# Performance work log

Measured on AMD Instinct MI355X. Metric: run time of the kernel, lower is better.

The kernel has to match this reference:

```python
import jax, jax.numpy as jnp
import numpy as np

B, S, D, H, E, K = 4, 1024, 1024, 4096, 8, 2

def setup_inputs() -> dict:
    key = jax.random.key(0)
    ks = jax.random.split(key, 6)
    sd = 1.0 / np.sqrt(D)
    sh = 1.0 / np.sqrt(H)
    return {
        "x": jax.random.normal(ks[0], (B, S, D), jnp.float32),
        "Wg": jax.random.normal(ks[1], (D, E), jnp.float32) * sd,
        "bg": jnp.zeros((E,), jnp.float32),
        "W1": jax.random.normal(ks[2], (E, D, H), jnp.float32) * sd,
        "b1": jnp.zeros((E, H), jnp.float32),
        "Wa": jax.random.normal(ks[3], (E, D, H), jnp.float32) * sd,
        "ba": jnp.zeros((E, H), jnp.float32),
        "W2": jax.random.normal(ks[4], (E, H, D), jnp.float32) * sh,
        "b2": jnp.zeros((E, D), jnp.float32),
        "kv_cache": 0,
    }

def reference(x, Wg, bg, W1, b1, Wa, ba, W2, b2, kv_cache):
    # gate: softmax over experts, top-k, renormalize
    gate = jax.nn.softmax(x @ Wg + bg, axis=-1)            # [B,S,E]
    w, idx = jax.lax.top_k(gate, K)                        # [B,S,K]
    w = w / jnp.sum(w, axis=-1, keepdims=True)
    # dense all-expert FF with SwiGLU: fc2( silu(fc_a(x)) * fc1(x) )
    a = jnp.einsum('bsd,edh->bseh', x, Wa) + ba            # [B,S,E,H]
    g = a * jax.nn.sigmoid(a)
    u = jnp.einsum('bsd,edh->bseh', x, W1) + b1
    y = jnp.einsum('bseh,ehd->bsed', g * u, W2) + b2       # [B,S,E,D]
    # gather top-k experts per token and combine
    sel = jnp.take_along_axis(y, idx[..., None], axis=2)   # [B,S,K,D]
    out = jnp.sum(sel * w[..., None], axis=-2)             # [B,S,D]
    return out
```

## Files before the change

### kernel.cpp

```cpp
#include <hip/hip_runtime.h>
#include <hip/hip_bf16.h>
#include <math.h>

#define TOKENS 4096
#define DD 1024
#define HH 4096
#define NE 8
#define PAIRS 8192
#define ROWCAP 8320
#define TILE_CAP 72

typedef __bf16 bf16x8 __attribute__((ext_vector_type(8)));
typedef float f32x4 __attribute__((ext_vector_type(4)));

__device__ __forceinline__ unsigned short f2bf(float f) {
  union { float f; unsigned int u; } c; c.f = f;
  unsigned int x = c.u;
  return (unsigned short)((x + 0x7fffu + ((x >> 16) & 1u)) >> 16);
}

__device__ __forceinline__ void lds16(void* l, const void* g) {
  __builtin_amdgcn_global_load_lds((const __attribute__((address_space(1))) void*)g,
                                   (__attribute__((address_space(3))) void*)l, 16, 0, 0);
}

__global__ void init_kernel(int* counts) {
  if (threadIdx.x < NE) counts[threadIdx.x] = 0;
}

__global__ __launch_bounds__(256) void transpose_kernel(const float* __restrict__ in,
                                                        unsigned short* __restrict__ out,
                                                        int R, int C) {
  int ntr = R >> 6, ntc = C >> 6;
  int per_e = ntr * ntc;
  int b = blockIdx.x;
  int e = b / per_e;
  int rem = b - e * per_e;
  int tr = rem / ntc, tc = rem - (rem / ntc) * ntc;
  const float* ie = in + (size_t)e * R * C;
  unsigned short* oe = out + (size_t)e * R * C;

  __shared__ float t[64][68];
  int tid = threadIdx.x;
  int lr = tid >> 2;
  int c4 = (tid & 3) << 4;
  const float* src = ie + (size_t)(tr * 64 + lr) * C + tc * 64 + c4;
  float4 v0 = *(const float4*)(src);
  float4 v1 = *(const float4*)(src + 4);
  float4 v2 = *(const float4*)(src + 8);
  float4 v3 = *(const float4*)(src + 12);
  *(float4*)&t[lr][c4] = v0;
  *(float4*)&t[lr][c4 + 4] = v1;
  *(float4*)&t[lr][c4 + 8] = v2;
  *(float4*)&t[lr][c4 + 12] = v3;
  __syncthreads();

  int oc = tid >> 2;
  int r0 = (tid & 3) << 4;
  unsigned int pk[8];
#pragma unroll
  for (int i = 0; i < 8; i++) {
    unsigned int lo = f2bf(t[r0 + 2 * i][oc]);
    unsigned int hi = f2bf(t[r0 + 2 * i + 1][oc]);
    pk[i] = lo | (hi << 16);
  }
  unsigned short* dst = oe + (size_t)(tc * 64 + oc) * R + tr * 64 + r0;
  *(uint4*)(dst) = make_uint4(pk[0], pk[1], pk[2], pk[3]);
  *(uint4*)(dst + 8) = make_uint4(pk[4], pk[5], pk[6], pk[7]);
}

__global__ __launch_bounds__(256) void gate_kernel(const float* __restrict__ x,
    const float* __restrict__ Wg, const float* __restrict__ bg,
    int* __restrict__ counts, int* __restrict__ tok_e, int* __restrict__ tok_slot,
    float* __restrict__ tok_w) {
  int t = blockIdx.x, tid = threadIdx.x;
  const float* xr = x + (size_t)t * DD;
  float p[8] = {0, 0, 0, 0, 0, 0, 0, 0};
  for (int d = tid; d < DD; d += 256) {
    float xv = xr[d];
    const float4* wrow = (const float4*)(Wg + (size_t)d * NE);
    float4 w0 = wrow[0], w1 = wrow[1];
    p[0] += xv * w0.x; p[1] += xv * w0.y; p[2] += xv * w0.z; p[3] += xv * w0.w;
    p[4] += xv * w1.x; p[5] += xv * w1.y; p[6] += xv * w1.z; p[7] += xv * w1.w;
  }
#pragma unroll
  for (int e = 0; e < 8; e++) {
    p[e] += __shfl_down(p[e], 32);
    p[e] += __shfl_down(p[e], 16);
    p[e] += __shfl_down(p[e], 8);
    p[e] += __shfl_down(p[e], 4);
    p[e] += __shfl_down(p[e], 2);
    p[e] += __shfl_down(p[e], 1);
  }
  __shared__ float red[4][8];
  if ((tid & 63) == 0) {
#pragma unroll
    for (int e = 0; e < 8; e++) red[tid >> 6][e] = p[e];
  }
  __syncthreads();
  if (tid == 0) {
    float l[8];
#pragma unroll
    for (int e = 0; e < 8; e++) l[e] = red[0][e] + red[1][e] + red[2][e] + red[3][e] + bg[e];
    int e0 = 0; float l0 = l[0];
    for (int e = 1; e < 8; e++) if (l[e] > l0) { e0 = e; l0 = l[e]; }
    int e1 = -1; float l1 = -3.4e38f;
    for (int e = 0; e < 8; e++) if (e != e0 && l[e] > l1) { e1 = e; l1 = l[e]; }
    float w0 = 1.f / (1.f + __expf(l1 - l0));
    float w1 = 1.f - w0;
    int s0 = atomicAdd(&counts[e0], 1);
    int s1 = atomicAdd(&counts[e1], 1);
    tok_e[2 * t] = e0;     tok_slot[2 * t] = s0;     tok_w[2 * t] = w0;
    tok_e[2 * t + 1] = e1; tok_slot[2 * t + 1] = s1; tok_w[2 * t + 1] = w1;
  }
}

__global__ void scan_kernel(const int* __restrict__ counts, int* __restrict__ offsets,
                            int* __restrict__ tm_e, int* __restrict__ tm_row0,
                            int* __restrict__ tm_nrow, int* __restrict__ ntp) {
  if (threadIdx.x != 0 || blockIdx.x != 0) return;
  int off = 0, nt = 0;
  for (int e = 0; e < NE; e++) {
    offsets[e] = off;
    int c = counts[e];
    for (int r = 0; r < c; r += 128) {
      tm_e[nt] = e;
      tm_row0[nt] = off + r;
      tm_nrow[nt] = (c - r < 128) ? (c - r) : 128;
      nt++;
    }
    off += c;
  }
  *ntp = nt;
}

__global__ __launch_bounds__(64) void gather_kernel(const float* __restrict__ x,
    const int* __restrict__ tok_e, const int* __restrict__ tok_slot,
    const float* __restrict__ tok_w, const int* __restrict__ offsets,
    unsigned short* __restrict__ Xe, int* __restrict__ pair_row, float* __restrict__ rw) {
  int pp = blockIdx.x, tid = threadIdx.x;
  int e = tok_e[pp];
  int row = offsets[e] + tok_slot[pp];
  int t = pp >> 1;
  const float* src = x + (size_t)t * DD + tid * 16;
  float4 v0 = *(const float4*)(src);
  float4 v1 = *(const float4*)(src + 4);
  float4 v2 = *(const float4*)(src + 8);
  float4 v3 = *(const float4*)(src + 12);
  unsigned int pk[8];
  pk[0] = f2bf(v0.x) | ((unsigned int)f2bf(v0.y) << 16);
  pk[1] = f2bf(v0.z) | ((unsigned int)f2bf(v0.w) << 16);
  pk[2] = f2bf(v1.x) | ((unsigned int)f2bf(v1.y) << 16);
  pk[3] = f2bf(v1.z) | ((unsigned int)f2bf(v1.w) << 16);
  pk[4] = f2bf(v2.x) | ((unsigned int)f2bf(v2.y) << 16);
  pk[5] = f2bf(v2.z) | ((unsigned int)f2bf(v2.w) << 16);
  pk[6] = f2bf(v3.x) | ((unsigned int)f2bf(v3.y) << 16);
  pk[7] = f2bf(v3.z) | ((unsigned int)f2bf(v3.w) << 16);
  unsigned short* dst = Xe + (size_t)row * DD + tid * 16;
  *(uint4*)(dst) = make_uint4(pk[0], pk[1], pk[2], pk[3]);
  *(uint4*)(dst + 8) = make_uint4(pk[4], pk[5], pk[6], pk[7]);
  if (tid == 0) { pair_row[pp] = row; rw[row] = tok_w[pp]; }
}

__global__ __launch_bounds__(256) void gemm1_kernel(
    const unsigned short* __restrict__ Xe,
    const unsigned short* __restrict__ WaT,
    const unsigned short* __restrict__ W1T,
    const float* __restrict__ ba, const float* __restrict__ b1,
    unsigned short* __restrict__ h,
    const int* __restrict__ tm_e, const int* __restrict__ tm_row0,
    const int* __restrict__ tm_nrow, const int* __restrict__ ntp) {
  int tile = blockIdx.x >> 6;
  if (tile >= *ntp) return;
  int n0 = (blockIdx.x & 63) << 6;
  int e = tm_e[tile], row0 = tm_row0[tile], nrow = tm_nrow[tile];

  __shared__ unsigned short lA[128 * 32];
  __shared__ unsigned short lBa[64 * 32];
  __shared__ unsigned short lBu[64 * 32];

  int tid = threadIdx.x;
  int lane = tid & 63, wid = tid >> 6;
  int wm = wid >> 1, wn = wid & 1;
  int fr = lane & 15, kc = lane >> 4;

  const unsigned short* gA = Xe + (size_t)row0 * DD;
  const unsigned short* gBa = WaT + ((size_t)e << 22) + (size_t)n0 * DD;
  const unsigned short* gBu = W1T + ((size_t)e << 22) + (size_t)n0 * DD;

  int ar0 = tid >> 2;
  int akc = (tid & 3) << 3;

  f32x4 accA[4][2], accU[4][2];
  f32x4 z = {0.f, 0.f, 0.f, 0.f};
#pragma unroll
  for (int m = 0; m < 4; m++)
#pragma unroll
    for (int n = 0; n < 2; n++) { accA[m][n] = z; accU[m][n] = z; }

  for (int k0 = 0; k0 < DD; k0 += 32) {
    lds16(lA + (size_t)tid * 8,        gA + (size_t)ar0 * DD + k0 + akc);
    lds16(lA + (size_t)(tid + 256) * 8, gA + (size_t)(ar0 + 64) * DD + k0 + akc);
    lds16(lBa + (size_t)tid * 8,       gBa + (size_t)ar0 * DD + k0 + akc);
    lds16(lBu + (size_t)tid * 8,       gBu + (size_t)ar0 * DD + k0 + akc);
    __syncthreads();
    bf16x8 a[4], bA[2], bU[2];
#pragma unroll
    for (int m = 0; m < 4; m++)
      a[m] = *(const bf16x8*)(lA + (wm * 64 + m * 16 + fr) * 32 + kc * 8);
#pragma unroll
    for (int n = 0; n < 2; n++) {
      bA[n] = *(const bf16x8*)(lBa + (wn * 32 + n * 16 + fr) * 32 + kc * 8);
      bU[n] = *(const bf16x8*)(lBu + (wn * 32 + n * 16 + fr) * 32 + kc * 8);
    }
#pragma unroll
    for (int m = 0; m < 4; m++)
#pragma unroll
      for (int n = 0; n < 2; n++) {
        accA[m][n] = __builtin_amdgcn_mfma_f32_16x16x32_bf16(a[m], bA[n], accA[m][n], 0, 0, 0);
        accU[m][n] = __builtin_amdgcn_mfma_f32_16x16x32_bf16(a[m], bU[n], accU[m][n], 0, 0, 0);
      }
    __syncthreads();
  }

  int lr4 = kc * 4;
#pragma unroll
  for (int n = 0; n < 2; n++) {
    int col = n0 + wn * 32 + n * 16 + fr;
    float bav = ba[e * HH + col];
    float buv = b1[e * HH + col];
#pragma unroll
    for (int m = 0; m < 4; m++) {
#pragma unroll
      for (int j = 0; j < 4; j++) {
        int r = wm * 64 + m * 16 + lr4 + j;
        if (r < nrow) {
          float av = accA[m][n][j] + bav;
          float uv = accU[m][n][j] + buv;
          float s = __builtin_amdgcn_rcpf(1.f + __expf(-av));
          float hv = av * s * uv;
          h[(size_t)(row0 + r) * HH + col] = f2bf(hv);
        }
      }
    }
  }
}

__global__ __launch_bounds__(256) void gemm2_kernel(
    const unsigned short* __restrict__ h,
    const unsigned short* __restrict__ W2T,
    const float* __restrict__ b2, const float* __restrict__ rw,
    float* __restrict__ contrib,
    const int* __restrict__ tm_e, const int* __restrict__ tm_row0,
    const int* __restrict__ tm_nrow, const int* __restrict__ ntp) {
  int tile = blockIdx.x >> 3;
  if (tile >= *ntp) return;
  int n0 = (blockIdx.x & 7) << 7;
  int e = tm_e[tile], row0 = tm_row0[tile], nrow = tm_nrow[tile];

  __shared__ unsigned short lA[128 * 32];
  __shared__ unsigned short lB[128 * 32];

  int tid = threadIdx.x;
  int lane = tid & 63, wid = tid >> 6;
  int wm = wid >> 1, wn = wid & 1;
  int fr = lane & 15, kc = lane >> 4;

  const unsigned short* gA = h + (size_t)row0 * HH;
  const unsigned short* gB = W2T + ((size_t)e << 22) + (size_t)n0 * HH;

  int ar0 = tid >> 2;
  int akc = (tid & 3) << 3;

  f32x4 acc[4][4];
  f32x4 z = {0.f, 0.f, 0.f, 0.f};
#pragma unroll
  for (int m = 0; m < 4; m++)
#pragma unroll
    for (int n = 0; n < 4; n++) acc[m][n] = z;

  for (int k0 = 0; k0 < HH; k0 += 32) {
    lds16(lA + (size_t)tid * 8,         gA + (size_t)ar0 * HH + k0 + akc);
    lds16(lA + (size_t)(tid + 256) * 8, gA + (size_t)(ar0 + 64) * HH + k0 + akc);
    lds16(lB + (size_t)tid * 8,         gB + (size_t)ar0 * HH + k0 + akc);
    lds16(lB + (size_t)(tid + 256) * 8, gB + (size_t)(ar0 + 64) * HH + k0 + akc);
    __syncthreads();
    bf16x8 a[4], b[4];
#pragma unroll
    for (int m = 0; m < 4; m++)
      a[m] = *(const bf16x8*)(lA + (wm * 64 + m * 16 + fr) * 32 + kc * 8);
#pragma unroll
    for (int n = 0; n < 4; n++)
      b[n] = *(const bf16x8*)(lB + (wn * 64 + n * 16 + fr) * 32 + kc * 8);
#pragma unroll
    for (int m = 0; m < 4; m++)
#pragma unroll
      for (int n = 0; n < 4; n++)
        acc[m][n] = __builtin_amdgcn_mfma_f32_16x16x32_bf16(a[m], b[n], acc[m][n], 0, 0, 0);
    __syncthreads();
  }

  float b2v[4];
#pragma unroll
  for (int n = 0; n < 4; n++) b2v[n] = b2[e * DD + n0 + wn * 64 + n * 16 + fr];
  int lr4 = kc * 4;
#pragma unroll
  for (int m = 0; m < 4; m++) {
#pragma unroll
    for (int j = 0; j < 4; j++) {
      int r = wm * 64 + m * 16 + lr4 + j;
      if (r < nrow) {
        float wv = rw[row0 + r];
        float* dst = contrib + (size_t)(row0 + r) * DD + n0 + wn * 64 + fr;
#pragma unroll
        for (int n = 0; n < 4; n++)
          dst[n * 16] = wv * (acc[m][n][j] + b2v[n]);
      }
    }
  }
}

__global__ __launch_bounds__(256) void combine_kernel(const float* __restrict__ contrib,
    const int* __restrict__ pair_row, float* __restrict__ out) {
  int t = blockIdx.x, tid = threadIdx.x;
  int r0 = pair_row[2 * t], r1 = pair_row[2 * t + 1];
  const float4* c0 = (const float4*)(contrib + (size_t)r0 * DD);
  const float4* c1 = (const float4*)(contrib + (size_t)r1 * DD);
  float4* o = (float4*)(out + (size_t)t * DD);
  float4 a = c0[tid], b = c1[tid];
  o[tid] = make_float4(a.x + b.x, a.y + b.y, a.z + b.z, a.w + b.w);
}

extern "C" void kernel_launch(void* const* d_in, const int* in_sizes, int n_in,
                              void* d_out, int out_size, void* d_ws, size_t ws_size,
                              hipStream_t stream) {
  const float* x  = (const float*)d_in[0];
  const float* Wg = (const float*)d_in[1];
  const float* bg = (const float*)d_in[2];
  const float* W1 = (const float*)d_in[3];
  const float* b1 = (const float*)d_in[4];
  const float* Wa = (const float*)d_in[5];
  const float* ba = (const float*)d_in[6];
  const float* W2 = (const float*)d_in[7];
  const float* b2 = (const float*)d_in[8];
  float* out = (float*)d_out;
  (void)in_sizes; (void)n_in; (void)out_size; (void)ws_size;

  char* p = (char*)d_ws;
  auto take = [&](size_t bytes) { char* r = p; p += (bytes + 255) & ~(size_t)255; return r; };
  unsigned short* WaT = (unsigned short*)take((size_t)NE * HH * DD * 2);
  unsigned short* W1T = (unsigned short*)take((size_t)NE * HH * DD * 2);
  unsigned short* W2T = (unsigned short*)take((size_t)NE * DD * HH * 2);
  unsigned short* Xe  = (unsigned short*)take((size_t)ROWCAP * DD * 2);
  unsigned short* hb  = (unsigned short*)take((size_t)ROWCAP * HH * 2);
  float* contrib      = (float*)take((size_t)ROWCAP * DD * 4);
  int* counts   = (int*)take(64);
  int* offsets  = (int*)take(64);
  int* tok_e    = (int*)take(PAIRS * 4);
  int* tok_slot = (int*)take(PAIRS * 4);
  float* tok_w  = (float*)take(PAIRS * 4);
  int* pair_row = (int*)take(PAIRS * 4);
  float* rw     = (float*)take(ROWCAP * 4);
  int* tm_e     = (int*)take(TILE_CAP * 4);
  int* tm_row0  = (int*)take(TILE_CAP * 4);
  int* tm_nrow  = (int*)take(TILE_CAP * 4);
  int* ntp      = (int*)take(64);

  init_kernel<<<1, 64, 0, stream>>>(counts);
  transpose_kernel<<<NE * 16 * 64, 256, 0, stream>>>(Wa, WaT, DD, HH);
  transpose_kernel<<<NE * 16 * 64, 256, 0, stream>>>(W1, W1T, DD, HH);
  transpose_kernel<<<NE * 64 * 16, 256, 0, stream>>>(W2, W2T, HH, DD);
  gate_kernel<<<TOKENS, 256, 0, stream>>>(x, Wg, bg, counts, tok_e, tok_slot, tok_w);
  scan_kernel<<<1, 64, 0, stream>>>(counts, offsets, tm_e, tm_row0, tm_nrow, ntp);
  gather_kernel<<<PAIRS, 64, 0, stream>>>(x, tok_e, tok_slot, tok_w, offsets, Xe, pair_row, rw);
  gemm1_kernel<<<TILE_CAP * 64, 256, 0, stream>>>(Xe, WaT, W1T, ba, b1, hb, tm_e, tm_row0, tm_nrow, ntp);
  gemm2_kernel<<<TILE_CAP * 8, 256, 0, stream>>>(hb, W2T, b2, rw, contrib, tm_e, tm_row0, tm_nrow, ntp);
  combine_kernel<<<TOKENS, 256, 0, stream>>>(contrib, pair_row, out);
}
```

Baseline: 563.4 us.

## Enlarge expert GEMM tiles to 256 rows with double-buffered LDS pipeline

Expert row tiles grow from 128 to 256 rows, and both grouped GEMMs move to 512-thread blocks. gemm1 now covers 128 output columns per block. Both kernels use two dynamic-LDS buffers so global-to-LDS loads for the next K step overlap MFMA work on the current one, with explicit waitcnt and barrier in place of __syncthreads. Block indices are remapped to group work across the grid for cache locality. The aims are more weight reuse per load and hidden load latency, at the cost of more padded rows on partial tiles, fewer blocks, and higher register and LDS use per block.

```diff
diff --git a/kernel.cpp b/kernel.cpp
--- a/kernel.cpp
+++ b/kernel.cpp
@@ -7,8 +7,8 @@
 #define HH 4096
 #define NE 8
 #define PAIRS 8192
-#define ROWCAP 8320
-#define TILE_CAP 72
+#define ROWCAP 8448
+#define TILE_CAP 40
 
 typedef __bf16 bf16x8 __attribute__((ext_vector_type(8)));
 typedef float f32x4 __attribute__((ext_vector_type(4)));
@@ -119,17 +119,19 @@
                             int* __restrict__ tm_e, int* __restrict__ tm_row0,
                             int* __restrict__ tm_nrow, int* __restrict__ ntp) {
   if (threadIdx.x != 0 || blockIdx.x != 0) return;
+  int c[NE];
+#pragma unroll
+  for (int e = 0; e < NE; e++) c[e] = counts[e];
   int off = 0, nt = 0;
   for (int e = 0; e < NE; e++) {
     offsets[e] = off;
-    int c = counts[e];
-    for (int r = 0; r < c; r += 128) {
+    for (int r = 0; r < c[e]; r += 256) {
       tm_e[nt] = e;
       tm_row0[nt] = off + r;
-      tm_nrow[nt] = (c - r < 128) ? (c - r) : 128;
+      tm_nrow[nt] = (c[e] - r < 256) ? (c[e] - r) : 256;
       nt++;
     }
-    off += c;
+    off += c[e];
   }
   *ntp = nt;
 }
@@ -162,7 +164,7 @@
   if (tid == 0) { pair_row[pp] = row; rw[row] = tok_w[pp]; }
 }
 
-__global__ __launch_bounds__(256) void gemm1_kernel(
+__global__ __launch_bounds__(512, 2) void gemm1_kernel(
     const unsigned short* __restrict__ Xe,
     const unsigned short* __restrict__ WaT,
     const unsigned short* __restrict__ W1T,
@@ -170,57 +172,65 @@
     unsigned short* __restrict__ h,
     const int* __restrict__ tm_e, const int* __restrict__ tm_row0,
     const int* __restrict__ tm_nrow, const int* __restrict__ ntp) {
-  int tile = blockIdx.x >> 6;
+  extern __shared__ unsigned short sm[];
+  int chunk = gridDim.x >> 3;
+  int work = (blockIdx.x & 7) * chunk + (blockIdx.x >> 3);
+  int tile = work >> 5;
   if (tile >= *ntp) return;
-  int n0 = (blockIdx.x & 63) << 6;
+  int n0 = (work & 31) << 7;
   int e = tm_e[tile], row0 = tm_row0[tile], nrow = tm_nrow[tile];
-
-  __shared__ unsigned short lA[128 * 32];
-  __shared__ unsigned short lBa[64 * 32];
-  __shared__ unsigned short lBu[64 * 32];
 
   int tid = threadIdx.x;
   int lane = tid & 63, wid = tid >> 6;
-  int wm = wid >> 1, wn = wid & 1;
+  int wm = wid >> 2, wn = wid & 3;
   int fr = lane & 15, kc = lane >> 4;
 
   const unsigned short* gA = Xe + (size_t)row0 * DD;
   const unsigned short* gBa = WaT + ((size_t)e << 22) + (size_t)n0 * DD;
   const unsigned short* gBu = W1T + ((size_t)e << 22) + (size_t)n0 * DD;
 
-  int ar0 = tid >> 2;
-  int akc = (tid & 3) << 3;
-
-  f32x4 accA[4][2], accU[4][2];
+  int sr = tid >> 2;
+  int sk = (tid & 3) << 3;
+
+  f32x4 accA[8][2], accU[8][2];
   f32x4 z = {0.f, 0.f, 0.f, 0.f};
 #pragma unroll
-  for (int m = 0; m < 4; m++)
+  for (int m = 0; m < 8; m++)
 #pragma unroll
     for (int n = 0; n < 2; n++) { accA[m][n] = z; accU[m][n] = z; }
 
-  for (int k0 = 0; k0 < DD; k0 += 32) {
-    lds16(lA + (size_t)tid * 8,        gA + (size_t)ar0 * DD + k0 + akc);
-    lds16(lA + (size_t)(tid + 256) * 8, gA + (size_t)(ar0 + 64) * DD + k0 + akc);
-    lds16(lBa + (size_t)tid * 8,       gBa + (size_t)ar0 * DD + k0 + akc);
-    lds16(lBu + (size_t)tid * 8,       gBu + (size_t)ar0 * DD + k0 + akc);
-    __syncthreads();
-    bf16x8 a[4], bA[2], bU[2];
-#pragma unroll
-    for (int m = 0; m < 4; m++)
-      a[m] = *(const bf16x8*)(lA + (wm * 64 + m * 16 + fr) * 32 + kc * 8);
+  auto stage = [&](int kt, int buf) {
+    int k0 = kt << 5;
+    unsigned short* L = sm + buf * 16384;
+    lds16(L + (size_t)tid * 8,         gA + (size_t)sr * DD + k0 + sk);
+    lds16(L + (size_t)(tid + 512) * 8, gA + (size_t)(sr + 128) * DD + k0 + sk);
+    lds16(L + 8192 + (size_t)tid * 8,  gBa + (size_t)sr * DD + k0 + sk);
+    lds16(L + 12288 + (size_t)tid * 8, gBu + (size_t)sr * DD + k0 + sk);
+  };
+
+  stage(0, 0);
+  for (int t = 0; t < 32; ++t) {
+    int nxt = (t + 1 < 32) ? t + 1 : 31;
+    stage(nxt, (t + 1) & 1);
+    asm volatile("s_waitcnt vmcnt(4)\ns_barrier" ::: "memory");
+    const unsigned short* L = sm + (t & 1) * 16384;
+    bf16x8 a[8], bA[2], bU[2];
+#pragma unroll
+    for (int m = 0; m < 8; m++)
+      a[m] = *(const bf16x8*)(L + (wm * 128 + m * 16 + fr) * 32 + kc * 8);
 #pragma unroll
     for (int n = 0; n < 2; n++) {
-      bA[n] = *(const bf16x8*)(lBa + (wn * 32 + n * 16 + fr) * 32 + kc * 8);
-      bU[n] = *(const bf16x8*)(lBu + (wn * 32 + n * 16 + fr) * 32 + kc * 8);
+      bA[n] = *(const bf16x8*)(L + 8192 + (wn * 32 + n * 16 + fr) * 32 + kc * 8);
+      bU[n] = *(const bf16x8*)(L + 12288 + (wn * 32 + n * 16 + fr) * 32 + kc * 8);
     }
 #pragma unroll
-    for (int m = 0; m < 4; m++)
+    for (int m = 0; m < 8; m++)
 #pragma unroll
       for (int n = 0; n < 2; n++) {
         accA[m][n] = __builtin_amdgcn_mfma_f32_16x16x32_bf16(a[m], bA[n], accA[m][n], 0, 0, 0);
         accU[m][n] = __builtin_amdgcn_mfma_f32_16x16x32_bf16(a[m], bU[n], accU[m][n], 0, 0, 0);
       }
-    __syncthreads();
+    asm volatile("s_waitcnt lgkmcnt(0)\ns_barrier" ::: "memory");
   }
 
   int lr4 = kc * 4;
@@ -230,10 +240,10 @@
     float bav = ba[e * HH + col];
     float buv = b1[e * HH + col];
 #pragma unroll
-    for (int m = 0; m < 4; m++) {
+    for (int m = 0; m < 8; m++) {
 #pragma unroll
       for (int j = 0; j < 4; j++) {
-        int r = wm * 64 + m * 16 + lr4 + j;
+        int r = wm * 128 + m * 16 + lr4 + j;
         if (r < nrow) {
           float av = accA[m][n][j] + bav;
           float uv = accU[m][n][j] + buv;
@@ -246,20 +256,20 @@
   }
 }
 
-__global__ __launch_bounds__(256) void gemm2_kernel(
+__global__ __launch_bounds__(512, 2) void gemm2_kernel(
     const unsigned short* __restrict__ h,
     const unsigned short* __restrict__ W2T,
     const float* __restrict__ b2, const float* __restrict__ rw,
     float* __restrict__ contrib,
     const int* __restrict__ tm_e, const int* __restrict__ tm_row0,
     const int* __restrict__ tm_nrow, const int* __restrict__ ntp) {
-  int tile = blockIdx.x >> 3;
+  extern __shared__ unsigned short sm[];
+  int chunk = gridDim.x >> 3;
+  int work = (blockIdx.x & 7) * chunk + (blockIdx.x >> 3);
+  int tile = work >> 3;
   if (tile >= *ntp) return;
-  int n0 = (blockIdx.x & 7) << 7;
+  int n0 = (work & 7) << 7;
   int e = tm_e[tile], row0 = tm_row0[tile], nrow = tm_nrow[tile];
-
-  __shared__ unsigned short lA[128 * 32];
-  __shared__ unsigned short lB[128 * 32];
 
   int tid = threadIdx.x;
   int lane = tid & 63, wid = tid >> 6;
@@ -269,8 +279,8 @@
   const unsigned short* gA = h + (size_t)row0 * HH;
   const unsigned short* gB = W2T + ((size_t)e << 22) + (size_t)n0 * HH;
 
-  int ar0 = tid >> 2;
-  int akc = (tid & 3) << 3;
+  int sr = tid >> 2;
+  int sk = (tid & 3) << 3;
 
   f32x4 acc[4][4];
   f32x4 z = {0.f, 0.f, 0.f, 0.f};
@@ -279,25 +289,33 @@
 #pragma unroll
     for (int n = 0; n < 4; n++) acc[m][n] = z;
 
-  for (int k0 = 0; k0 < HH; k0 += 32) {
-    lds16(lA + (size_t)tid * 8,         gA + (size_t)ar0 * HH + k0 + akc);
-    lds16(lA + (size_t)(tid + 256) * 8, gA + (size_t)(ar0 + 64) * HH + k0 + akc);
-    lds16(lB + (size_t)tid * 8,         gB + (size_t)ar0 * HH + k0 + akc);
-    lds16(lB + (size_t)(tid + 256) * 8, gB + (size_t)(ar0 + 64) * HH + k0 + akc);
-    __syncthreads();
+  auto stage = [&](int kt, int buf) {
+    int k0 = kt << 5;
+    unsigned short* L = sm + buf * 12288;
+    lds16(L + (size_t)tid * 8,         gA + (size_t)sr * HH + k0 + sk);
+    lds16(L + (size_t)(tid + 512) * 8, gA + (size_t)(sr + 128) * HH + k0 + sk);
+    lds16(L + 8192 + (size_t)tid * 8,  gB + (size_t)sr * HH + k0 + sk);
+  };
+
+  stage(0, 0);
+  for (int t = 0; t < 128; ++t) {
+    int nxt = (t + 1 < 128) ? t + 1 : 127;
+    stage(nxt, (t + 1) & 1);
+    asm volatile("s_waitcnt vmcnt(3)\ns_barrier" ::: "memory");
+    const unsigned short* L = sm + (t & 1) * 12288;
     bf16x8 a[4], b[4];
 #pragma unroll
     for (int m = 0; m < 4; m++)
-      a[m] = *(const bf16x8*)(lA + (wm * 64 + m * 16 + fr) * 32 + kc * 8);
+      a[m] = *(const bf16x8*)(L + (wm * 64 + m * 16 + fr) * 32 + kc * 8);
 #pragma unroll
     for (int n = 0; n < 4; n++)
-      b[n] = *(const bf16x8*)(lB + (wn * 64 + n * 16 + fr) * 32 + kc * 8);
+      b[n] = *(const bf16x8*)(L + 8192 + (wn * 64 + n * 16 + fr) * 32 + kc * 8);
 #pragma unroll
     for (int m = 0; m < 4; m++)
 #pragma unroll
       for (int n = 0; n < 4; n++)
         acc[m][n] = __builtin_amdgcn_mfma_f32_16x16x32_bf16(a[m], b[n], acc[m][n], 0, 0, 0);
-    __syncthreads();
+    asm volatile("s_waitcnt lgkmcnt(0)\ns_barrier" ::: "memory");
   }
 
   float b2v[4];
@@ -373,7 +391,7 @@
   gate_kernel<<<TOKENS, 256, 0, stream>>>(x, Wg, bg, counts, tok_e, tok_slot, tok_w);
   scan_kernel<<<1, 64, 0, stream>>>(counts, offsets, tm_e, tm_row0, tm_nrow, ntp);
   gather_kernel<<<PAIRS, 64, 0, stream>>>(x, tok_e, tok_slot, tok_w, offsets, Xe, pair_row, rw);
-  gemm1_kernel<<<TILE_CAP * 64, 256, 0, stream>>>(Xe, WaT, W1T, ba, b1, hb, tm_e, tm_row0, tm_nrow, ntp);
-  gemm2_kernel<<<TILE_CAP * 8, 256, 0, stream>>>(hb, W2T, b2, rw, contrib, tm_e, tm_row0, tm_nrow, ntp);
+  gemm1_kernel<<<TILE_CAP * 32, 512, 64 * 1024, stream>>>(Xe, WaT, W1T, ba, b1, hb, tm_e, tm_row0, tm_nrow, ntp);
+  gemm2_kernel<<<TILE_CAP * 8, 512, 48 * 1024, stream>>>(hb, W2T, b2, rw, contrib, tm_e, tm_row0, tm_nrow, ntp);
   combine_kernel<<<TOKENS, 256, 0, stream>>>(contrib, pair_row, out);
 }
```

New measurement: 586.3 us. 1.04x slower.

## Double-buffer LDS with XOR swizzle in grouped GEMMs and merge weight transposes

Applied to the files above, without the earlier changes.

Both grouped GEMM kernels now use two LDS buffers, so the global-to-LDS load for the next K step is issued before the MFMA work on the current one. This removes the load-then-wait stall at each step. The LDS layout gets an XOR swizzle on the K chunk to reduce bank conflicts on the fragment reads. The three weight-transpose launches are merged into one launch, and ROWCAP is enlarged to cover the padded reads near tile ends; the price is one extra redundant stage load per tile and twice the LDS per block.

```diff
diff --git a/kernel.cpp b/kernel.cpp
--- a/kernel.cpp
+++ b/kernel.cpp
@@ -7,8 +7,10 @@
 #define HH 4096
 #define NE 8
 #define PAIRS 8192
-#define ROWCAP 8320
-#define TILE_CAP 72
+#define ROWCAP 8448
+#define TCAP 72
+#define G1_NT 32
+#define G2_NT 128
 
 typedef __bf16 bf16x8 __attribute__((ext_vector_type(8)));
 typedef float f32x4 __attribute__((ext_vector_type(4)));
@@ -28,14 +30,21 @@
   if (threadIdx.x < NE) counts[threadIdx.x] = 0;
 }
 
-__global__ __launch_bounds__(256) void transpose_kernel(const float* __restrict__ in,
-                                                        unsigned short* __restrict__ out,
-                                                        int R, int C) {
+__global__ __launch_bounds__(256) void transpose_kernel(
+    const float* __restrict__ Wa, const float* __restrict__ W1, const float* __restrict__ W2,
+    unsigned short* __restrict__ WaT, unsigned short* __restrict__ W1T,
+    unsigned short* __restrict__ W2T) {
+  int b = blockIdx.x;
+  int sec = b >> 13;
+  int sb = b & 8191;
+  const float* in; unsigned short* out; int R, C;
+  if (sec == 0)      { in = Wa; out = WaT; R = DD; C = HH; }
+  else if (sec == 1) { in = W1; out = W1T; R = DD; C = HH; }
+  else               { in = W2; out = W2T; R = HH; C = DD; }
   int ntr = R >> 6, ntc = C >> 6;
   int per_e = ntr * ntc;
-  int b = blockIdx.x;
-  int e = b / per_e;
-  int rem = b - e * per_e;
+  int e = sb / per_e;
+  int rem = sb - e * per_e;
   int tr = rem / ntc, tc = rem - (rem / ntc) * ntc;
   const float* ie = in + (size_t)e * R * C;
   unsigned short* oe = out + (size_t)e * R * C;
@@ -119,17 +128,18 @@
                             int* __restrict__ tm_e, int* __restrict__ tm_row0,
                             int* __restrict__ tm_nrow, int* __restrict__ ntp) {
   if (threadIdx.x != 0 || blockIdx.x != 0) return;
+  int c[NE];
+#pragma unroll
+  for (int e = 0; e < NE; e++) c[e] = counts[e];
   int off = 0, nt = 0;
   for (int e = 0; e < NE; e++) {
     offsets[e] = off;
-    int c = counts[e];
-    for (int r = 0; r < c; r += 128) {
-      tm_e[nt] = e;
-      tm_row0[nt] = off + r;
-      tm_nrow[nt] = (c - r < 128) ? (c - r) : 128;
+    for (int r = 0; r < c[e]; r += 128) {
+      tm_e[nt] = e; tm_row0[nt] = off + r;
+      tm_nrow[nt] = (c[e] - r < 128) ? (c[e] - r) : 128;
       nt++;
     }
-    off += c;
+    off += c[e];
   }
   *ntp = nt;
 }
@@ -162,6 +172,7 @@
   if (tid == 0) { pair_row[pp] = row; rw[row] = tok_w[pp]; }
 }
 
+
 __global__ __launch_bounds__(256) void gemm1_kernel(
     const unsigned short* __restrict__ Xe,
     const unsigned short* __restrict__ WaT,
@@ -170,26 +181,41 @@
     unsigned short* __restrict__ h,
     const int* __restrict__ tm_e, const int* __restrict__ tm_row0,
     const int* __restrict__ tm_nrow, const int* __restrict__ ntp) {
-  int tile = blockIdx.x >> 6;
+  __shared__ unsigned short sm[2][8192];
+
+  int work = blockIdx.x;
+  int tile = work >> 6;
   if (tile >= *ntp) return;
-  int n0 = (blockIdx.x & 63) << 6;
+  int n0 = (work & 63) << 6;
   int e = tm_e[tile], row0 = tm_row0[tile], nrow = tm_nrow[tile];
-
-  __shared__ unsigned short lA[128 * 32];
-  __shared__ unsigned short lBa[64 * 32];
-  __shared__ unsigned short lBu[64 * 32];
 
   int tid = threadIdx.x;
   int lane = tid & 63, wid = tid >> 6;
   int wm = wid >> 1, wn = wid & 1;
   int fr = lane & 15, kc = lane >> 4;
 
-  const unsigned short* gA = Xe + (size_t)row0 * DD;
-  const unsigned short* gBa = WaT + ((size_t)e << 22) + (size_t)n0 * DD;
-  const unsigned short* gBu = W1T + ((size_t)e << 22) + (size_t)n0 * DD;
-
-  int ar0 = tid >> 2;
-  int akc = (tid & 3) << 3;
+  int srow = tid >> 2;
+  int cd = tid & 3;
+  int scl = (cd ^ ((srow >> 1) & 3)) << 3;
+
+  const unsigned short* pA0 = Xe + (size_t)(row0 + srow) * DD + scl;
+  const unsigned short* pA1 = Xe + (size_t)(row0 + 64 + srow) * DD + scl;
+  const unsigned short* pBa = WaT + ((size_t)e << 22) + (size_t)(n0 + srow) * DD + scl;
+  const unsigned short* pBu = W1T + ((size_t)e << 22) + (size_t)(n0 + srow) * DD + scl;
+
+  unsigned short* ldst = &sm[0][0] + (size_t)tid * 8;
+
+  int aof[4], bof[2];
+#pragma unroll
+  for (int m = 0; m < 4; m++) {
+    int r = wm * 64 + m * 16 + fr;
+    aof[m] = r * 64 + ((kc ^ ((r >> 1) & 3)) << 4);
+  }
+#pragma unroll
+  for (int n = 0; n < 2; n++) {
+    int r = wn * 32 + n * 16 + fr;
+    bof[n] = 8192 + r * 64 + ((kc ^ ((r >> 1) & 3)) << 4);
+  }
 
   f32x4 accA[4][2], accU[4][2];
   f32x4 z = {0.f, 0.f, 0.f, 0.f};
@@ -198,20 +224,28 @@
 #pragma unroll
     for (int n = 0; n < 2; n++) { accA[m][n] = z; accU[m][n] = z; }
 
-  for (int k0 = 0; k0 < DD; k0 += 32) {
-    lds16(lA + (size_t)tid * 8,        gA + (size_t)ar0 * DD + k0 + akc);
-    lds16(lA + (size_t)(tid + 256) * 8, gA + (size_t)(ar0 + 64) * DD + k0 + akc);
-    lds16(lBa + (size_t)tid * 8,       gBa + (size_t)ar0 * DD + k0 + akc);
-    lds16(lBu + (size_t)tid * 8,       gBu + (size_t)ar0 * DD + k0 + akc);
-    __syncthreads();
+  auto stage = [&](int T, int buf) {
+    int koff = (T < G1_NT ? T : G1_NT - 1) << 5;
+    unsigned short* L = ldst + buf * 8192;
+    lds16(L, pA0 + koff);
+    lds16(L + 2048, pA1 + koff);
+    lds16(L + 4096, pBa + koff);
+    lds16(L + 6144, pBu + koff);
+  };
+
+  stage(0, 0);
+  __syncthreads();
+  int buf = 0;
+  for (int T = 0; T < G1_NT; ++T) {
+    stage(T + 1, buf ^ 1);
+    const char* lb = (const char*)&sm[0][0] + (buf << 14);
     bf16x8 a[4], bA[2], bU[2];
 #pragma unroll
-    for (int m = 0; m < 4; m++)
-      a[m] = *(const bf16x8*)(lA + (wm * 64 + m * 16 + fr) * 32 + kc * 8);
+    for (int m = 0; m < 4; m++) a[m] = *(const bf16x8*)(lb + aof[m]);
 #pragma unroll
     for (int n = 0; n < 2; n++) {
-      bA[n] = *(const bf16x8*)(lBa + (wn * 32 + n * 16 + fr) * 32 + kc * 8);
-      bU[n] = *(const bf16x8*)(lBu + (wn * 32 + n * 16 + fr) * 32 + kc * 8);
+      bA[n] = *(const bf16x8*)(lb + bof[n]);
+      bU[n] = *(const bf16x8*)(lb + bof[n] + 4096);
     }
 #pragma unroll
     for (int m = 0; m < 4; m++)
@@ -221,6 +255,7 @@
         accU[m][n] = __builtin_amdgcn_mfma_f32_16x16x32_bf16(a[m], bU[n], accU[m][n], 0, 0, 0);
       }
     __syncthreads();
+    buf ^= 1;
   }
 
   int lr4 = kc * 4;
@@ -238,8 +273,7 @@
           float av = accA[m][n][j] + bav;
           float uv = accU[m][n][j] + buv;
           float s = __builtin_amdgcn_rcpf(1.f + __expf(-av));
-          float hv = av * s * uv;
-          h[(size_t)(row0 + r) * HH + col] = f2bf(hv);
+          h[(size_t)(row0 + r) * HH + col] = f2bf(av * s * uv);
         }
       }
     }
@@ -247,30 +281,47 @@
 }
 
 __global__ __launch_bounds__(256) void gemm2_kernel(
-    const unsigned short* __restrict__ h,
+    const unsigned short* __restrict__ hb,
     const unsigned short* __restrict__ W2T,
     const float* __restrict__ b2, const float* __restrict__ rw,
     float* __restrict__ contrib,
     const int* __restrict__ tm_e, const int* __restrict__ tm_row0,
     const int* __restrict__ tm_nrow, const int* __restrict__ ntp) {
-  int tile = blockIdx.x >> 3;
+  __shared__ unsigned short sm[2][8192];
+
+  int work = blockIdx.x;
+  int tile = work >> 3;
   if (tile >= *ntp) return;
-  int n0 = (blockIdx.x & 7) << 7;
+  int n0 = (work & 7) << 7;
   int e = tm_e[tile], row0 = tm_row0[tile], nrow = tm_nrow[tile];
-
-  __shared__ unsigned short lA[128 * 32];
-  __shared__ unsigned short lB[128 * 32];
 
   int tid = threadIdx.x;
   int lane = tid & 63, wid = tid >> 6;
   int wm = wid >> 1, wn = wid & 1;
   int fr = lane & 15, kc = lane >> 4;
 
-  const unsigned short* gA = h + (size_t)row0 * HH;
-  const unsigned short* gB = W2T + ((size_t)e << 22) + (size_t)n0 * HH;
-
-  int ar0 = tid >> 2;
-  int akc = (tid & 3) << 3;
+  int srow = tid >> 2;
+  int cd = tid & 3;
+  int scl = (cd ^ ((srow >> 1) & 3)) << 3;
+
+  const unsigned short* pA0 = hb + (size_t)(row0 + srow) * HH + scl;
+  const unsigned short* pA1 = hb + (size_t)(row0 + 64 + srow) * HH + scl;
+  const unsigned short* pB0 = W2T + ((size_t)e << 22) + (size_t)(n0 + srow) * HH + scl;
+  const unsigned short* pB1 = W2T + ((size_t)e << 22) + (size_t)(n0 + 64 + srow) * HH + scl;
+
+  unsigned short* ldst = &sm[0][0] + (size_t)tid * 8;
+
+  int aof[4], bof[4];
+#pragma unroll
+  for (int m = 0; m < 4; m++) {
+    int r = wm * 64 + m * 16 + fr;
+    aof[m] = r * 64 + ((kc ^ ((r >> 1) & 3)) << 4);
+  }
+#pragma unroll
+  for (int n = 0; n < 4; n++) {
+    int r = wn * 64 + n * 16 + fr;
+    bof[n] = 8192 + r * 64 + ((kc ^ ((r >> 1) & 3)) << 4);
+  }
 
   f32x4 acc[4][4];
   f32x4 z = {0.f, 0.f, 0.f, 0.f};
@@ -279,25 +330,33 @@
 #pragma unroll
     for (int n = 0; n < 4; n++) acc[m][n] = z;
 
-  for (int k0 = 0; k0 < HH; k0 += 32) {
-    lds16(lA + (size_t)tid * 8,         gA + (size_t)ar0 * HH + k0 + akc);
-    lds16(lA + (size_t)(tid + 256) * 8, gA + (size_t)(ar0 + 64) * HH + k0 + akc);
-    lds16(lB + (size_t)tid * 8,         gB + (size_t)ar0 * HH + k0 + akc);
-    lds16(lB + (size_t)(tid + 256) * 8, gB + (size_t)(ar0 + 64) * HH + k0 + akc);
-    __syncthreads();
+  auto stage = [&](int T, int buf) {
+    int koff = (T < G2_NT ? T : G2_NT - 1) << 5;
+    unsigned short* L = ldst + buf * 8192;
+    lds16(L, pA0 + koff);
+    lds16(L + 2048, pA1 + koff);
+    lds16(L + 4096, pB0 + koff);
+    lds16(L + 6144, pB1 + koff);
+  };
+
+  stage(0, 0);
+  __syncthreads();
+  int buf = 0;
+  for (int T = 0; T < G2_NT; ++T) {
+    stage(T + 1, buf ^ 1);
+    const char* lb = (const char*)&sm[0][0] + (buf << 14);
     bf16x8 a[4], b[4];
 #pragma unroll
-    for (int m = 0; m < 4; m++)
-      a[m] = *(const bf16x8*)(lA + (wm * 64 + m * 16 + fr) * 32 + kc * 8);
-#pragma unroll
-    for (int n = 0; n < 4; n++)
-      b[n] = *(const bf16x8*)(lB + (wn * 64 + n * 16 + fr) * 32 + kc * 8);
+    for (int m = 0; m < 4; m++) a[m] = *(const bf16x8*)(lb + aof[m]);
+#pragma unroll
+    for (int n = 0; n < 4; n++) b[n] = *(const bf16x8*)(lb + bof[n]);
 #pragma unroll
     for (int m = 0; m < 4; m++)
 #pragma unroll
       for (int n = 0; n < 4; n++)
         acc[m][n] = __builtin_amdgcn_mfma_f32_16x16x32_bf16(a[m], b[n], acc[m][n], 0, 0, 0);
     __syncthreads();
+    buf ^= 1;
   }
 
   float b2v[4];
@@ -361,19 +420,17 @@
   float* tok_w  = (float*)take(PAIRS * 4);
   int* pair_row = (int*)take(PAIRS * 4);
   float* rw     = (float*)take(ROWCAP * 4);
-  int* tm_e     = (int*)take(TILE_CAP * 4);
-  int* tm_row0  = (int*)take(TILE_CAP * 4);
-  int* tm_nrow  = (int*)take(TILE_CAP * 4);
+  int* tm_e     = (int*)take(TCAP * 4);
+  int* tm_row0  = (int*)take(TCAP * 4);
+  int* tm_nrow  = (int*)take(TCAP * 4);
   int* ntp      = (int*)take(64);
 
   init_kernel<<<1, 64, 0, stream>>>(counts);
-  transpose_kernel<<<NE * 16 * 64, 256, 0, stream>>>(Wa, WaT, DD, HH);
-  transpose_kernel<<<NE * 16 * 64, 256, 0, stream>>>(W1, W1T, DD, HH);
-  transpose_kernel<<<NE * 64 * 16, 256, 0, stream>>>(W2, W2T, HH, DD);
+  transpose_kernel<<<3 * 8192, 256, 0, stream>>>(Wa, W1, W2, WaT, W1T, W2T);
   gate_kernel<<<TOKENS, 256, 0, stream>>>(x, Wg, bg, counts, tok_e, tok_slot, tok_w);
   scan_kernel<<<1, 64, 0, stream>>>(counts, offsets, tm_e, tm_row0, tm_nrow, ntp);
   gather_kernel<<<PAIRS, 64, 0, stream>>>(x, tok_e, tok_slot, tok_w, offsets, Xe, pair_row, rw);
-  gemm1_kernel<<<TILE_CAP * 64, 256, 0, stream>>>(Xe, WaT, W1T, ba, b1, hb, tm_e, tm_row0, tm_nrow, ntp);
-  gemm2_kernel<<<TILE_CAP * 8, 256, 0, stream>>>(hb, W2T, b2, rw, contrib, tm_e, tm_row0, tm_nrow, ntp);
+  gemm1_kernel<<<TCAP * 64, 256, 0, stream>>>(Xe, WaT, W1T, ba, b1, hb, tm_e, tm_row0, tm_nrow, ntp);
+  gemm2_kernel<<<TCAP * 8, 256, 0, stream>>>(hb, W2T, b2, rw, contrib, tm_e, tm_row0, tm_nrow, ntp);
   combine_kernel<<<TOKENS, 256, 0, stream>>>(contrib, pair_row, out);
 }
```

Result: no change. 556.8 us (-1.2%).
